# Performance work log

Measured on AMD Instinct MI355X. Metric: run time of the kernel, lower is better.

The kernel has to match this reference:

```python
import jax, jax.numpy as jnp
import numpy as np

EMBED_DIM = 128
NUM_CLASSES = 2
NUM_NODES = 100000
NUM_EDGES = 500000


def setup_inputs() -> dict:
    key = jax.random.key(0)
    k1, k2, k3, k4, k5, k6 = jax.random.split(key, 6)
    node_embed = jax.random.normal(k1, (NUM_NODES, EMBED_DIM), dtype=jnp.float32)
    edge_index = jax.random.randint(k2, (2, NUM_EDGES), 0, NUM_NODES, dtype=jnp.int64)
    # MLP params (torch Linear default init scale ~ 1/sqrt(fan_in))
    s1 = 1.0 / np.sqrt(2 * EMBED_DIM)
    s2 = 1.0 / np.sqrt(EMBED_DIM)
    W1 = jax.random.uniform(k3, (2 * EMBED_DIM, EMBED_DIM), jnp.float32, -s1, s1)
    b1 = jax.random.uniform(k4, (EMBED_DIM,), jnp.float32, -s1, s1)
    W2 = jax.random.uniform(k5, (EMBED_DIM, NUM_CLASSES), jnp.float32, -s2, s2)
    b2 = jax.random.uniform(k6, (NUM_CLASSES,), jnp.float32, -s2, s2)
    return {"node_embed": node_embed, "edge_index": edge_index,
            "W1": W1, "b1": b1, "W2": W2, "b2": b2}


def reference(node_embed, edge_index, W1, b1, W2, b2):
    row, col = edge_index[0], edge_index[1]
    # Gather endpoint embeddings and concat -> [num_edges, 2*embed_dim]
    edge_feat = jnp.concatenate([node_embed[row], node_embed[col]], axis=1)
    h = jax.nn.relu(edge_feat @ W1 + b1)  # [num_edges, embed_dim]
    # Dropout(0.1) is identity in eval mode.
    return h @ W2 + b2  # [num_edges, num_classes]
```

## Files before the change

kernel.cpp:

```cpp
#include <hip/hip_runtime.h>
#include <hip/hip_bf16.h>


#define EMBED 128

typedef _Float16 half8 __attribute__((ext_vector_type(8)));
typedef _Float16 half4 __attribute__((ext_vector_type(4)));
typedef float floatx4 __attribute__((ext_vector_type(4)));

__global__ __launch_bounds__(256) void prep(
    const float* __restrict__ W1, const float* __restrict__ W2,
    const float* __restrict__ b1, const int* __restrict__ idx,
    _Float16* __restrict__ WT, _Float16* __restrict__ W2PT,
    _Float16* __restrict__ b1f, int* __restrict__ flag) {
    if (blockIdx.x < 128) {
        __shared__ float lds[16][17];
        const int ty = threadIdx.x >> 4, tx = threadIdx.x & 15;
        const int r0 = (blockIdx.x >> 3) * 16;
        const int c0 = (blockIdx.x & 7) * 16;
        lds[ty][tx] = W1[(r0 + ty) * 128 + c0 + tx];
        __syncthreads();
        const int jbase = c0 + (r0 >= 128 ? 128 : 0);
        const int kbase = r0 & 127;
        WT[(size_t)(jbase + ty) * 128 + kbase + tx] = (_Float16)lds[tx][ty];
    } else {
        const int t = threadIdx.x;
        if (t < 64) {
            const int hw = idx[2 * t + 1];
            const unsigned long long m = __ballot(hw != 0);
            if (t == 0) *flag = (m == 0ull) ? 1 : 0;
        }
        if (t < 128) b1f[t] = (_Float16)b1[t];
        for (int i = t; i < 2048; i += 256) {
            const int n = i >> 7, k = i & 127;
            W2PT[i] = (n < 2) ? (_Float16)W2[k * 2 + n] : (_Float16)0.f;
        }
    }
}

__global__ __launch_bounds__(256) void gemm_ab(
    const float* __restrict__ X, const _Float16* __restrict__ WT,
    _Float16* __restrict__ AB, int n_nodes, int n_tiles) {
    __shared__ _Float16 sh[64 * 264];
    _Float16* xs   = sh;
    _Float16* outs = sh;
    const int t = threadIdx.x;
    const int w = t >> 6, lane = t & 63, lm = lane & 15, quad = lane >> 4;

    for (int T = blockIdx.x; T < n_tiles; T += gridDim.x) {
        const int mblk = T * 64;

#pragma unroll
        for (int i = 0; i < 8; ++i) {
            const int flat = i * 1024 + t * 4;
            const int row = flat >> 7, col = flat & 127;
            int node = mblk + row;
            if (node > n_nodes - 1) node = n_nodes - 1;
            const float4 v = *(const float4*)(X + (size_t)node * EMBED + col);
            half4 h;
            h[0] = (_Float16)v.x; h[1] = (_Float16)v.y;
            h[2] = (_Float16)v.z; h[3] = (_Float16)v.w;
            *(half4*)(xs + row * 136 + col) = h;
        }
        __syncthreads();

        floatx4 acc[4][4];
#pragma unroll
        for (int a = 0; a < 4; ++a)
#pragma unroll
            for (int b = 0; b < 4; ++b)
                acc[a][b] = (floatx4){0.f, 0.f, 0.f, 0.f};

#pragma unroll
        for (int ks = 0; ks < 4; ++ks) {
            const int k0 = ks * 32 + quad * 8;
            half8 xf[4];
#pragma unroll
            for (int mf = 0; mf < 4; ++mf)
                xf[mf] = *(const half8*)(xs + (mf * 16 + lm) * 136 + k0);
#pragma unroll
            for (int jf = 0; jf < 4; ++jf) {
                const int j = w * 64 + jf * 16 + lm;
                const half8 wf = *(const half8*)(WT + (size_t)j * EMBED + k0);
#pragma unroll
                for (int mf = 0; mf < 4; ++mf)
                    acc[mf][jf] = __builtin_amdgcn_mfma_f32_16x16x32_f16(wf, xf[mf], acc[mf][jf], 0, 0, 0);
            }
        }
        __syncthreads();

#pragma unroll
        for (int mf = 0; mf < 4; ++mf) {
#pragma unroll
            for (int jf = 0; jf < 4; ++jf) {
                half4 h;
#pragma unroll
                for (int r = 0; r < 4; ++r) h[r] = (_Float16)acc[mf][jf][r];
                *(half4*)(outs + (mf * 16 + lm) * 264 + w * 64 + jf * 16 + quad * 4) = h;
            }
        }
        __syncthreads();

#pragma unroll
        for (int i = 0; i < 8; ++i) {
            const int idx8 = i * 256 + t;
            const int node = idx8 >> 5, jj = idx8 & 31;
            if (mblk + node < n_nodes)
                *(half8*)(AB + (size_t)(mblk + node) * 256 + jj * 8) =
                    *(const half8*)(outs + node * 264 + jj * 8);
        }
        __syncthreads();
    }
}

__global__ __launch_bounds__(256) void edge_mlp(
    const _Float16* __restrict__ AB, const int* __restrict__ eidx,
    const int* __restrict__ flag, const _Float16* __restrict__ b1f,
    const _Float16* __restrict__ W2PT, const float* __restrict__ b2,
    float* __restrict__ out, int n_edges) {
    const int lane = threadIdx.x & 63, lm = lane & 15, quad = lane >> 4;
    const int ebase = (blockIdx.x * 4 + (threadIdx.x >> 6)) * 32;
    if (ebase >= n_edges) return;

    const int mode = *flag;
    int e0 = ebase + lm, e1 = ebase + 16 + lm;
    if (e0 > n_edges - 1) e0 = n_edges - 1;
    if (e1 > n_edges - 1) e1 = n_edges - 1;
    int row0, col0, row1, col1;
    if (mode) {
        row0 = eidx[2 * (size_t)e0];
        col0 = eidx[2 * ((size_t)n_edges + e0)];
        row1 = eidx[2 * (size_t)e1];
        col1 = eidx[2 * ((size_t)n_edges + e1)];
    } else {
        row0 = eidx[e0];
        col0 = eidx[(size_t)n_edges + e0];
        row1 = eidx[e1];
        col1 = eidx[(size_t)n_edges + e1];
    }

    const _Float16* a0p = AB + (size_t)row0 * 256;
    const _Float16* b0p = AB + (size_t)col0 * 256 + 128;
    const _Float16* a1p = AB + (size_t)row1 * 256;
    const _Float16* b1p = AB + (size_t)col1 * 256 + 128;

    half8 a0[4], b0[4], a1[4], b1[4];
#pragma unroll
    for (int ks = 0; ks < 4; ++ks) {
        const int k0 = ks * 32 + quad * 8;
        a0[ks] = *(const half8*)(a0p + k0);
        b0[ks] = *(const half8*)(b0p + k0);
        a1[ks] = *(const half8*)(a1p + k0);
        b1[ks] = *(const half8*)(b1p + k0);
    }

    floatx4 acc0 = (floatx4){0.f, 0.f, 0.f, 0.f};
    floatx4 acc1 = (floatx4){0.f, 0.f, 0.f, 0.f};
#pragma unroll
    for (int ks = 0; ks < 4; ++ks) {
        const int k0 = ks * 32 + quad * 8;
        const half8 bi = *(const half8*)(b1f + k0);
        const half8 wv = *(const half8*)(W2PT + lm * 128 + k0);
        half8 h0 = a0[ks] + b0[ks] + bi;
        half8 h1 = a1[ks] + b1[ks] + bi;
#pragma unroll
        for (int j = 0; j < 8; ++j) {
            h0[j] = h0[j] > (_Float16)0.f ? h0[j] : (_Float16)0.f;
            h1[j] = h1[j] > (_Float16)0.f ? h1[j] : (_Float16)0.f;
        }
        acc0 = __builtin_amdgcn_mfma_f32_16x16x32_f16(h0, wv, acc0, 0, 0, 0);
        acc1 = __builtin_amdgcn_mfma_f32_16x16x32_f16(h1, wv, acc1, 0, 0, 0);
    }

    if (lm < 2) {
        const float b2v = b2[lm];
#pragma unroll
        for (int r = 0; r < 4; ++r) {
            const int ed0 = ebase + quad * 4 + r;
            const int ed1 = ebase + 16 + quad * 4 + r;
            if (ed0 < n_edges) out[(size_t)ed0 * 2 + lm] = acc0[r] + b2v;
            if (ed1 < n_edges) out[(size_t)ed1 * 2 + lm] = acc1[r] + b2v;
        }
    }
}

extern "C" void kernel_launch(void* const* d_in, const int* in_sizes, int n_in,
                              void* d_out, int out_size, void* d_ws, size_t ws_size,
                              hipStream_t stream) {
    const float* X   = (const float*)d_in[0];
    const int*   idx = (const int*)d_in[1];
    const float* W1  = (const float*)d_in[2];
    const float* b1  = (const float*)d_in[3];
    const float* W2  = (const float*)d_in[4];
    const float* b2  = (const float*)d_in[5];
    float* out = (float*)d_out;

    const int n_nodes = in_sizes[0] / EMBED;
    const int n_edges = in_sizes[1] / 2;

    char* ws = (char*)d_ws;
    int*      flag = (int*)ws;
    _Float16* AB   = (_Float16*)(ws + 256);
    _Float16* WT   = (_Float16*)(ws + 256 + (size_t)n_nodes * 512);
    _Float16* W2PT = WT + 256 * 128;
    _Float16* b1f  = W2PT + 16 * 128;

    const int n_tiles = (n_nodes + 63) / 64;

    prep<<<129, 256, 0, stream>>>(W1, W2, b1, idx, WT, W2PT, b1f, flag);
    gemm_ab<<<n_tiles, 256, 0, stream>>>(X, WT, AB, n_nodes, n_tiles);
    edge_mlp<<<(n_edges + 127) / 128, 256, 0, stream>>>(
        AB, idx, flag, b1f, W2PT, b2, out, n_edges);
}
```

Baseline: 156.3 us.

## Register-prefetch next node tile in persistent gemm_ab loop

Turns gemm_ab into a persistent kernel with a fixed grid of 782 blocks. Each block now loads the X tile for its next iteration into registers while the MFMA work on the current tile runs, so global load latency overlaps with compute. The cost is more register pressure from 8 float4 prefetch buffers, which may reduce occupancy, and a hard-coded grid size that is tuned to this problem size.

```diff
diff --git a/kernel.cpp b/kernel.cpp
--- a/kernel.cpp
+++ b/kernel.cpp
@@ -47,22 +47,46 @@
     const int t = threadIdx.x;
     const int w = t >> 6, lane = t & 63, lm = lane & 15, quad = lane >> 4;
 
-    for (int T = blockIdx.x; T < n_tiles; T += gridDim.x) {
+    int srow[8], scol[8];
+#pragma unroll
+    for (int i = 0; i < 8; ++i) {
+        const int flat = i * 1024 + t * 4;
+        srow[i] = flat >> 7;
+        scol[i] = flat & 127;
+    }
+
+    int T = blockIdx.x;
+    float4 pf[8];
+    if (T < n_tiles) {
+#pragma unroll
+        for (int i = 0; i < 8; ++i) {
+            int node = T * 64 + srow[i];
+            if (node > n_nodes - 1) node = n_nodes - 1;
+            pf[i] = *(const float4*)(X + (size_t)node * EMBED + scol[i]);
+        }
+    }
+
+    for (; T < n_tiles; T += gridDim.x) {
         const int mblk = T * 64;
 
 #pragma unroll
         for (int i = 0; i < 8; ++i) {
-            const int flat = i * 1024 + t * 4;
-            const int row = flat >> 7, col = flat & 127;
-            int node = mblk + row;
-            if (node > n_nodes - 1) node = n_nodes - 1;
-            const float4 v = *(const float4*)(X + (size_t)node * EMBED + col);
             half4 h;
-            h[0] = (_Float16)v.x; h[1] = (_Float16)v.y;
-            h[2] = (_Float16)v.z; h[3] = (_Float16)v.w;
-            *(half4*)(xs + row * 136 + col) = h;
-        }
-        __syncthreads();
+            h[0] = (_Float16)pf[i].x; h[1] = (_Float16)pf[i].y;
+            h[2] = (_Float16)pf[i].z; h[3] = (_Float16)pf[i].w;
+            *(half4*)(xs + srow[i] * 136 + scol[i]) = h;
+        }
+        __syncthreads();
+
+        const int Tn = T + gridDim.x;
+        if (Tn < n_tiles) {
+#pragma unroll
+            for (int i = 0; i < 8; ++i) {
+                int node = Tn * 64 + srow[i];
+                if (node > n_nodes - 1) node = n_nodes - 1;
+                pf[i] = *(const float4*)(X + (size_t)node * EMBED + scol[i]);
+            }
+        }
 
         floatx4 acc[4][4];
 #pragma unroll
@@ -208,7 +232,7 @@
     const int n_tiles = (n_nodes + 63) / 64;
 
     prep<<<129, 256, 0, stream>>>(W1, W2, b1, idx, WT, W2PT, b1f, flag);
-    gemm_ab<<<n_tiles, 256, 0, stream>>>(X, WT, AB, n_nodes, n_tiles);
+    gemm_ab<<<782, 256, 0, stream>>>(X, WT, AB, n_nodes, n_tiles);
     edge_mlp<<<(n_edges + 127) / 128, 256, 0, stream>>>(
         AB, idx, flag, b1f, W2PT, b2, out, n_edges);
 }
```

Result: no change. 153.4 us (-1.9%).
